# Kernel optimization log

Hardware: AMD Instinct MI355X
Metric: run time of the kernel (lower is better)

Reference implementation:

```python
import jax, jax.numpy as jnp
import numpy as np

B, Q, N, C = 2, 1024, 4096, 768
H, D, REL = 12, 64, 32
SCALE = 1.0 / np.sqrt(D)


def _lin_coords(n_out, n_in):
    # align_corners=True mapping: x_in = x_out * (n_in-1)/(n_out-1)
    pos = jnp.arange(n_out, dtype=jnp.float32) * ((n_in - 1) / (n_out - 1))
    lo = jnp.clip(jnp.floor(pos).astype(jnp.int32), 0, n_in - 1)
    hi = jnp.clip(lo + 1, 0, n_in - 1)
    w = pos - lo.astype(jnp.float32)
    return lo, hi, w


def _interp_bias(bias, q_len, n_len):
    # bias: [H, 32, 32] -> [H, q_len, n_len] bilinear, align_corners=True
    lq, hq, wq = _lin_coords(q_len, REL)
    ln, hn, wn = _lin_coords(n_len, REL)
    b1 = bias[:, lq, :] * (1.0 - wq)[None, :, None] + bias[:, hq, :] * wq[None, :, None]  # [H,q,32]
    b2 = b1[:, :, ln] * (1.0 - wn)[None, None, :] + b1[:, :, hn] * wn[None, None, :]      # [H,q,n]
    return b2


def setup_inputs() -> dict:
    key = jax.random.key(0)
    ks = jax.random.split(key, 11)
    s = 1.0 / np.sqrt(C)
    return {
        "query": jax.random.normal(ks[0], (B, Q, C), jnp.float32),
        "key_value": jax.random.normal(ks[1], (B, N, C), jnp.float32),
        "Wq": jax.random.normal(ks[2], (C, C), jnp.float32) * s,
        "bq": jax.random.normal(ks[3], (C,), jnp.float32) * 0.01,
        "Wk": jax.random.normal(ks[4], (C, C), jnp.float32) * s,
        "bk": jax.random.normal(ks[5], (C,), jnp.float32) * 0.01,
        "Wv": jax.random.normal(ks[6], (C, C), jnp.float32) * s,
        "bv": jax.random.normal(ks[7], (C,), jnp.float32) * 0.01,
        "Wo": jax.random.normal(ks[8], (C, C), jnp.float32) * s,
        "bo": jax.random.normal(ks[9], (C,), jnp.float32) * 0.01,
        "rel_pos_bias": jax.random.normal(ks[10], (H, REL, REL), jnp.float32) * 0.02,
    }


def reference(query, key_value, Wq, bq, Wk, bk, Wv, bv, Wo, bo, rel_pos_bias):
    b, n, c = key_value.shape
    q_len = query.shape[1]
    # projections (dropout in eval mode -> identity)
    q = (query @ Wq + bq).reshape(b, q_len, H, D).transpose(0, 2, 1, 3)      # [B,H,Q,D]
    k = (key_value @ Wk + bk).reshape(b, n, H, D).transpose(0, 2, 1, 3)      # [B,H,N,D]
    v = (key_value @ Wv + bv).reshape(b, n, H, D).transpose(0, 2, 1, 3)      # [B,H,N,D]
    attn = jnp.einsum('bhqd,bhnd->bhqn', q, k) * SCALE
    attn = attn + _interp_bias(rel_pos_bias, q_len, n)[None]                 # [B,H,Q,N]
    p = jax.nn.softmax(attn, axis=-1)
    out = jnp.einsum('bhqn,bhnd->bhqd', p, v)
    out = out.transpose(0, 2, 1, 3).reshape(b, q_len, c)
    return out @ Wo + bo
```

## Files before the change

kernel.cpp:

```cpp
#include <hip/hip_runtime.h>
#include <stdint.h>

typedef unsigned short ushort_t;
typedef __bf16 bf16x8 __attribute__((ext_vector_type(8)));
typedef float f32x4 __attribute__((ext_vector_type(4)));
typedef unsigned short us4 __attribute__((ext_vector_type(4)));

#define LOG2E 1.4426950408889634f
#define NEG8L (-11.541560327111707f)
#define QSCALE 0.18033688011110974f

__device__ __forceinline__ ushort_t f2b(float f) {
    unsigned u = __float_as_uint(f);
    unsigned r = (u + 0x7fffu + ((u >> 16) & 1u)) >> 16;
    return (ushort_t)r;
}
__device__ __forceinline__ void gld16(const void* g, void* l) {
    __builtin_amdgcn_global_load_lds(
        (__attribute__((address_space(1))) void*)g,
        (__attribute__((address_space(3))) void*)l,
        16, 0, 0);
}

__global__ __launch_bounds__(256) void prep(
        const float* __restrict__ query, const float* __restrict__ keyv,
        const float* __restrict__ Wq, const float* __restrict__ Wk,
        const float* __restrict__ Wv, const float* __restrict__ Wo,
        const float* __restrict__ rel,
        ushort_t* __restrict__ qc, ushort_t* __restrict__ kvc,
        ushort_t* __restrict__ wtq, ushort_t* __restrict__ wtk,
        ushort_t* __restrict__ wtv, ushort_t* __restrict__ wto,
        ushort_t* __restrict__ b1b, ushort_t* __restrict__ wtab) {
    __shared__ ushort_t tsh[32][33];
    const int bid = blockIdx.x, tid = threadIdx.x;
    if (bid < 7680) {
        const float* src = (bid < 1536) ? query : keyv;
        ushort_t* dst = (bid < 1536) ? qc : kvc;
        int i = ((bid < 1536) ? bid : bid - 1536) * 256 + tid;
        float4 x = ((const float4*)src)[i];
        us4 v; v.x = f2b(x.x); v.y = f2b(x.y); v.z = f2b(x.z); v.w = f2b(x.w);
        ((us4*)dst)[i] = v;
    } else if (bid < 9984) {
        int t = bid - 7680, w = t / 576, tt = t - w * 576;
        const float* in = (w == 0) ? Wq : (w == 1) ? Wk : (w == 2) ? Wv : Wo;
        ushort_t* out = (w == 0) ? wtq : (w == 1) ? wtk : (w == 2) ? wtv : wto;
        int x = tid & 31, y = tid >> 5;
        int bx = (tt % 24) * 32, by = (tt / 24) * 32;
#pragma unroll
        for (int j = 0; j < 32; j += 8)
            tsh[y + j][x] = f2b(in[(size_t)(by + y + j) * 768 + bx + x]);
        __syncthreads();
#pragma unroll
        for (int j = 0; j < 32; j += 8)
            out[(size_t)(bx + y + j) * 768 + by + x] = tsh[x][y + j];
    } else if (bid < 11520) {
        int idx = (bid - 9984) * 256 + tid;
        int j = idx & 31, q = (idx >> 5) & 1023, h = idx >> 15;
        float pos = q * (31.0f / 1023.0f);
        float fl = floorf(pos);
        int lo = (int)fl; if (lo > 31) lo = 31;
        float w = pos - fl;
        int hi = lo + 1; if (hi > 31) hi = 31;
        float vlo = rel[(h * 32 + lo) * 32 + j];
        float vhi = rel[(h * 32 + hi) * 32 + j];
        b1b[idx] = f2b((vlo + (vhi - vlo) * w) * LOG2E);
    } else {
        int n = (bid - 11520) * 256 + tid;
        float pos = n * (31.0f / 4095.0f);
        float fl = floorf(pos);
        int ln = (int)fl; if (ln > 31) ln = 31;
        float wn = pos - fl;
        int hn = ln + 1; if (hn > 31) hn = 31;
        float vals[32];
#pragma unroll
        for (int j = 0; j < 32; ++j) vals[j] = 0.f;
        vals[ln] += 1.0f - wn;
        vals[hn] += wn;
#pragma unroll
        for (int j = 0; j < 32; ++j) wtab[n * 32 + j] = f2b(vals[j]);
    }
}

template <int MBC>
__device__ __forceinline__ void gemm_body(const ushort_t* __restrict__ A,
                                          const ushort_t* __restrict__ Bt,
                                          const float* __restrict__ bias,
                                          void* __restrict__ out,
                                          int mode, int lsh, float scale,
                                          int m0, int n0,
                                          ushort_t* As, ushort_t* Bs, int tid) {
    const int wave = tid >> 6, lane = tid & 63;
    const int quad = lane >> 4, l15 = lane & 15;
    const f32x4 z4 = {0.f, 0.f, 0.f, 0.f};
    f32x4 acc[MBC][4];
#pragma unroll
    for (int i = 0; i < MBC; ++i)
#pragma unroll
        for (int j = 0; j < 4; ++j) acc[i][j] = z4;

    const int lrow = lane >> 2;
    const int kswz = ((lane & 3) ^ (lrow & 3)) * 8;

    for (int kk = 0; kk < 768; kk += 32) {
        __syncthreads();
#pragma unroll
        for (int i = 0; i < MBC; ++i) {
            int c = wave * MBC + i;
            gld16(A + (size_t)(m0 + c * 16 + lrow) * 768 + kk + kswz, (void*)(As + c * 512));
        }
        gld16(Bt + (size_t)(n0 + wave * 16 + lrow) * 768 + kk + kswz, (void*)(Bs + wave * 512));
        __syncthreads();
        bf16x8 af[MBC], bf[4];
#pragma unroll
        for (int mb = 0; mb < MBC; ++mb) {
            int r = wave * 16 * MBC + mb * 16 + l15;
            af[mb] = *(const bf16x8*)(As + r * 32 + ((quad ^ (r & 3)) * 8));
        }
#pragma unroll
        for (int nb = 0; nb < 4; ++nb) {
            int r = nb * 16 + l15;
            bf[nb] = *(const bf16x8*)(Bs + r * 32 + ((quad ^ (r & 3)) * 8));
        }
#pragma unroll
        for (int mb = 0; mb < MBC; ++mb)
#pragma unroll
            for (int nb = 0; nb < 4; ++nb)
                acc[mb][nb] = __builtin_amdgcn_mfma_f32_16x16x32_bf16(af[mb], bf[nb], acc[mb][nb], 0, 0, 0);
    }

#pragma unroll
    for (int mb = 0; mb < MBC; ++mb) {
        int mbase = m0 + wave * 16 * MBC + mb * 16 + quad * 4;
#pragma unroll
        for (int nb = 0; nb < 4; ++nb) {
            int n = n0 + nb * 16 + l15;
            float bvf = bias[n];
            f32x4 a = acc[mb][nb];
            if (mode == 0) {
#pragma unroll
                for (int r = 0; r < 4; ++r)
                    ((float*)out)[(size_t)(mbase + r) * 768 + n] = (a[r] + bvf) * scale;
            } else if (mode == 1) {
                int h = n >> 6, d = n & 63;
#pragma unroll
                for (int r = 0; r < 4; ++r) {
                    int m = mbase + r;
                    int b = m >> lsh, l = m & ((1 << lsh) - 1);
                    ((ushort_t*)out)[((size_t)(((b * 12 + h) << lsh) + l) << 6) + d] = f2b((a[r] + bvf) * scale);
                }
            } else {
                int h = n >> 6, d = n & 63;
                int b = mbase >> lsh, l = mbase & ((1 << lsh) - 1);
                us4 v;
                v.x = f2b((a[0] + bvf) * scale);
                v.y = f2b((a[1] + bvf) * scale);
                v.z = f2b((a[2] + bvf) * scale);
                v.w = f2b((a[3] + bvf) * scale);
                *(us4*)((ushort_t*)out + ((size_t)((b * 12 + h) * 64 + d) << lsh) + l) = v;
            }
        }
    }
}

__global__ __launch_bounds__(256) void proj3(const ushort_t* __restrict__ qc,
                                             const ushort_t* __restrict__ kvc,
                                             const ushort_t* __restrict__ wtq,
                                             const ushort_t* __restrict__ wtk,
                                             const ushort_t* __restrict__ wtv,
                                             const float* __restrict__ bq,
                                             const float* __restrict__ bk,
                                             const float* __restrict__ bv,
                                             ushort_t* __restrict__ qp,
                                             ushort_t* __restrict__ kp,
                                             ushort_t* __restrict__ vtp) {
    __shared__ __align__(16) ushort_t As[128 * 32];
    __shared__ __align__(16) ushort_t Bs[64 * 32];
    const int bid = blockIdx.x, tid = threadIdx.x;
    if (bid < 384) {
        int mt = bid / 12, nt = bid - mt * 12;
        gemm_body<1>(qc, wtq, bq, qp, 1, 10, QSCALE, mt * 64, nt * 64, As, Bs, tid);
    } else if (bid < 1152) {
        int t = bid - 384, mt = t / 12, nt = t - mt * 12;
        gemm_body<2>(kvc, wtk, bk, kp, 1, 12, 1.0f, mt * 128, nt * 64, As, Bs, tid);
    } else {
        int t = bid - 1152, mt = t / 12, nt = t - mt * 12;
        gemm_body<2>(kvc, wtv, bv, vtp, 2, 12, 1.0f, mt * 128, nt * 64, As, Bs, tid);
    }
}

__global__ __launch_bounds__(256) void gemm_out(const ushort_t* __restrict__ ab,
                                                const ushort_t* __restrict__ wto,
                                                const float* __restrict__ bo,
                                                float* __restrict__ out) {
    __shared__ __align__(16) ushort_t As[64 * 32];
    __shared__ __align__(16) ushort_t Bs[64 * 32];
    const int bid = blockIdx.x, tid = threadIdx.x;
    int mt = bid / 12, nt = bid - mt * 12;
    gemm_body<1>(ab, wto, bo, out, 0, 0, 1.0f, mt * 64, nt * 64, As, Bs, tid);
}

__global__ __launch_bounds__(256) void attn64s(const ushort_t* __restrict__ qp,
                                               const ushort_t* __restrict__ kp,
                                               const ushort_t* __restrict__ vt,
                                               const ushort_t* __restrict__ b1b,
                                               const ushort_t* __restrict__ wtab,
                                               float* __restrict__ po,
                                               float* __restrict__ pl) {
    __shared__ __align__(16) ushort_t k_s[64 * 64];
    __shared__ __align__(16) ushort_t v_s[64 * 64];
    __shared__ __align__(16) float pf[4][576];

    const int tid = threadIdx.x;
    const int wave = tid >> 6, lane = tid & 63;
    const int quad = lane >> 4, l15 = lane & 15;
    const int qt = blockIdx.x, h = blockIdx.y, z = blockIdx.z;
    const int b = z >> 2, sp = z & 3;
    const int q0 = qt * 64;
    const int bh = b * 12 + h;

    const ushort_t* qg = qp + ((size_t)bh * 1024 + q0) * 64;
    const ushort_t* kg = kp + (size_t)bh * 4096 * 64;
    const ushort_t* vg = vt + (size_t)bh * 64 * 4096;

    const int rowq = wave * 16 + l15;
    bf16x8 aq[2];
#pragma unroll
    for (int ks = 0; ks < 2; ++ks)
        aq[ks] = *(const bf16x8*)(qg + (size_t)rowq * 64 + (ks * 4 + quad) * 8);
    bf16x8 ab1 = *(const bf16x8*)(b1b + ((size_t)(h * 1024 + q0 + rowq)) * 32 + quad * 8);

    const f32x4 mC = {NEG8L, NEG8L, NEG8L, NEG8L};
    const f32x4 z4 = {0.f, 0.f, 0.f, 0.f};
    f32x4 o[4];
    float lsum[4];
#pragma unroll
    for (int d = 0; d < 4; ++d) o[d] = z4;
#pragma unroll
    for (int r = 0; r < 4; ++r) lsum[r] = 0.f;

    const int arow = lane >> 3;
    const int ablk = lane & 7;

    for (int nt = 0; nt < 16; ++nt) {
        const int n0 = sp * 1024 + nt * 64;
        __syncthreads();
#pragma unroll
        for (int i = 0; i < 2; ++i) {
            int c = wave * 2 + i;
            int row = c * 8 + arow;
            int k16 = ablk ^ (row & 7);
            gld16(kg + (size_t)(n0 + row) * 64 + k16 * 8, (void*)(k_s + c * 512));
            gld16(vg + (size_t)row * 4096 + n0 + k16 * 8, (void*)(v_s + c * 512));
        }
        __syncthreads();

        bf16x8 wf[4];
#pragma unroll
        for (int nb = 0; nb < 4; ++nb)
            wf[nb] = *(const bf16x8*)(wtab + (size_t)(n0 + nb * 16 + l15) * 32 + quad * 8);

        f32x4 s[4];
#pragma unroll
        for (int nb = 0; nb < 4; ++nb) {
            s[nb] = __builtin_amdgcn_mfma_f32_16x16x32_bf16(ab1, wf[nb], mC, 0, 0, 0);
#pragma unroll
            for (int ks = 0; ks < 2; ++ks) {
                int rn = nb * 16 + l15;
                bf16x8 bk = *(const bf16x8*)(k_s + rn * 64 + (((ks * 4 + quad) ^ (rn & 7)) * 8));
                s[nb] = __builtin_amdgcn_mfma_f32_16x16x32_bf16(aq[ks], bk, s[nb], 0, 0, 0);
            }
        }
#pragma unroll
        for (int nb = 0; nb < 4; ++nb)
#pragma unroll
            for (int r = 0; r < 4; ++r) {
                float p = exp2f(s[nb][r]);
                s[nb][r] = p;
                lsum[r] += p;
            }
#pragma unroll
        for (int p = 0; p < 2; ++p) {
#pragma unroll
            for (int i = 0; i < 2; ++i) {
                int nb = 2 * p + i;
                float* dst = &pf[wave][(i * 16 + l15) * 18 + quad * 4];
                *(float2*)dst = make_float2(s[nb][0], s[nb][1]);
                *(float2*)(dst + 2) = make_float2(s[nb][2], s[nb][3]);
            }
            bf16x8 ap;
#pragma unroll
            for (int j = 0; j < 8; ++j)
                ap[j] = (__bf16)pf[wave][(quad * 8 + j) * 18 + l15];
#pragma unroll
            for (int d = 0; d < 4; ++d) {
                int rd = d * 16 + l15;
                bf16x8 bv = *(const bf16x8*)(v_s + rd * 64 + (((p * 4 + quad) ^ (rd & 7)) * 8));
                o[d] = __builtin_amdgcn_mfma_f32_16x16x32_bf16(ap, bv, o[d], 0, 0, 0);
            }
        }
    }

#pragma unroll
    for (int r = 0; r < 4; ++r)
#pragma unroll
        for (int off = 1; off < 16; off <<= 1)
            lsum[r] += __shfl_xor(lsum[r], off, 64);

    const size_t pbase = ((size_t)(sp * 24 + bh)) * 1024;
#pragma unroll
    for (int r = 0; r < 4; ++r) {
        int qrow = q0 + wave * 16 + quad * 4 + r;
        if (l15 == 0) pl[pbase + qrow] = lsum[r];
#pragma unroll
        for (int d = 0; d < 4; ++d)
            po[(pbase + qrow) * 64 + d * 16 + l15] = o[d][r];
    }
}

__global__ __launch_bounds__(256) void combine(const float* __restrict__ po,
                                               const float* __restrict__ pl,
                                               ushort_t* __restrict__ ab) {
    int idx = blockIdx.x * 256 + threadIdx.x;
    int e = idx * 4;
    int b = e / 786432;
    int rem = e - b * 786432;
    int q = rem / 768;
    int col = rem - q * 768;
    int h = col >> 6, d = col & 63;
    int bh = b * 12 + h;
    float4 acc = {0.f, 0.f, 0.f, 0.f};
    float l = 0.f;
#pragma unroll
    for (int s = 0; s < 4; ++s) {
        size_t base = ((size_t)(s * 24 + bh)) * 1024 + q;
        float4 v = *(const float4*)(po + base * 64 + d);
        acc.x += v.x; acc.y += v.y; acc.z += v.z; acc.w += v.w;
        l += pl[base];
    }
    float inv = 1.0f / l;
    us4 v;
    v.x = f2b(acc.x * inv); v.y = f2b(acc.y * inv);
    v.z = f2b(acc.z * inv); v.w = f2b(acc.w * inv);
    *(us4*)(ab + (size_t)(b * 1024 + q) * 768 + col) = v;
}

extern "C" void kernel_launch(void* const* d_in, const int* in_sizes, int n_in,
                              void* d_out, int out_size, void* d_ws, size_t ws_size,
                              hipStream_t stream) {
    const float* query = (const float*)d_in[0];
    const float* keyv  = (const float*)d_in[1];
    const float* Wq = (const float*)d_in[2];
    const float* bq = (const float*)d_in[3];
    const float* Wk = (const float*)d_in[4];
    const float* bk = (const float*)d_in[5];
    const float* Wv = (const float*)d_in[6];
    const float* bv = (const float*)d_in[7];
    const float* Wo = (const float*)d_in[8];
    const float* bo = (const float*)d_in[9];
    const float* rel = (const float*)d_in[10];

    char* ws = (char*)d_ws;
    ushort_t* qc   = (ushort_t*)(ws + 0);
    ushort_t* kvc  = (ushort_t*)(ws + 3145728);
    ushort_t* wtq  = (ushort_t*)(ws + 15728640);
    ushort_t* wtk  = (ushort_t*)(ws + 16908288);
    ushort_t* wtv  = (ushort_t*)(ws + 18087936);
    ushort_t* wto  = (ushort_t*)(ws + 19267584);
    ushort_t* qp   = (ushort_t*)(ws + 20447232);
    ushort_t* kp   = (ushort_t*)(ws + 23592960);
    ushort_t* vtp  = (ushort_t*)(ws + 36175872);
    ushort_t* b1b  = (ushort_t*)(ws + 48758784);
    ushort_t* wtab = (ushort_t*)(ws + 49545216);
    ushort_t* ab   = (ushort_t*)(ws + 49807360);
    float*    po   = (float*)(ws + 52953088);
    float*    pl   = (float*)(ws + 78118912);

    prep<<<11536, 256, 0, stream>>>(query, keyv, Wq, Wk, Wv, Wo, rel,
                                    qc, kvc, wtq, wtk, wtv, wto, b1b, wtab);
    proj3<<<1920, 256, 0, stream>>>(qc, kvc, wtq, wtk, wtv, bq, bk, bv, qp, kp, vtp);
    attn64s<<<dim3(16, 12, 8), 256, 0, stream>>>(qp, kp, vtp, b1b, wtab, po, pl);
    combine<<<1536, 256, 0, stream>>>(po, pl, ab);
    gemm_out<<<384, 256, 0, stream>>>(ab, wto, bo, (float*)d_out);
}
```

Measured before the change: 232.9 us.

## Enlarge projection and attention tiles to 128 and store P as bf16

```diff
diff --git a/kernel.cpp b/kernel.cpp
--- a/kernel.cpp
+++ b/kernel.cpp
@@ -81,40 +81,117 @@
     }
 }
 
-template <int MBC>
-__device__ __forceinline__ void gemm_body(const ushort_t* __restrict__ A,
-                                          const ushort_t* __restrict__ Bt,
-                                          const float* __restrict__ bias,
-                                          void* __restrict__ out,
-                                          int mode, int lsh, float scale,
-                                          int m0, int n0,
-                                          ushort_t* As, ushort_t* Bs, int tid) {
+__device__ __forceinline__ void gemm_store(float bvf, f32x4 a, void* out,
+                                           int mode, int lsh, float scale,
+                                           int mbase, int n) {
+    if (mode == 0) {
+#pragma unroll
+        for (int r = 0; r < 4; ++r)
+            ((float*)out)[(size_t)(mbase + r) * 768 + n] = (a[r] + bvf) * scale;
+    } else if (mode == 1) {
+        int h = n >> 6, d = n & 63;
+#pragma unroll
+        for (int r = 0; r < 4; ++r) {
+            int m = mbase + r;
+            int b = m >> lsh, l = m & ((1 << lsh) - 1);
+            ((ushort_t*)out)[((size_t)(((b * 12 + h) << lsh) + l) << 6) + d] = f2b((a[r] + bvf) * scale);
+        }
+    } else {
+        int h = n >> 6, d = n & 63;
+        int b = mbase >> lsh, l = mbase & ((1 << lsh) - 1);
+        us4 v;
+        v.x = f2b((a[0] + bvf) * scale);
+        v.y = f2b((a[1] + bvf) * scale);
+        v.z = f2b((a[2] + bvf) * scale);
+        v.w = f2b((a[3] + bvf) * scale);
+        *(us4*)((ushort_t*)out + ((size_t)((b * 12 + h) * 64 + d) << lsh) + l) = v;
+    }
+}
+
+__device__ __forceinline__ void gemm_body128(const ushort_t* __restrict__ A,
+                                             const ushort_t* __restrict__ Bt,
+                                             const float* __restrict__ bias,
+                                             void* __restrict__ out,
+                                             int mode, int lsh, float scale,
+                                             int m0, int n0,
+                                             ushort_t* As, ushort_t* Bs, int tid) {
+    const int wave = tid >> 6, lane = tid & 63;
+    const int quad = lane >> 4, l15 = lane & 15;
+    const int wm = wave >> 1, wn = wave & 1;
+    const f32x4 z4 = {0.f, 0.f, 0.f, 0.f};
+    f32x4 acc[4][4];
+#pragma unroll
+    for (int i = 0; i < 4; ++i)
+#pragma unroll
+        for (int j = 0; j < 4; ++j) acc[i][j] = z4;
+
+    const int lrow = lane >> 2;
+    const int kswz = ((lane & 3) ^ (lrow & 3)) * 8;
+
+    for (int kk = 0; kk < 768; kk += 32) {
+        __syncthreads();
+#pragma unroll
+        for (int i = 0; i < 2; ++i) {
+            int c = wave * 2 + i;
+            gld16(A + (size_t)(m0 + c * 16 + lrow) * 768 + kk + kswz, (void*)(As + c * 512));
+            gld16(Bt + (size_t)(n0 + c * 16 + lrow) * 768 + kk + kswz, (void*)(Bs + c * 512));
+        }
+        __syncthreads();
+        bf16x8 af[4], bf[4];
+#pragma unroll
+        for (int mb = 0; mb < 4; ++mb) {
+            int r = wm * 64 + mb * 16 + l15;
+            af[mb] = *(const bf16x8*)(As + r * 32 + ((quad ^ (r & 3)) * 8));
+        }
+#pragma unroll
+        for (int nb = 0; nb < 4; ++nb) {
+            int r = wn * 64 + nb * 16 + l15;
+            bf[nb] = *(const bf16x8*)(Bs + r * 32 + ((quad ^ (r & 3)) * 8));
+        }
+#pragma unroll
+        for (int mb = 0; mb < 4; ++mb)
+#pragma unroll
+            for (int nb = 0; nb < 4; ++nb)
+                acc[mb][nb] = __builtin_amdgcn_mfma_f32_16x16x32_bf16(af[mb], bf[nb], acc[mb][nb], 0, 0, 0);
+    }
+
+#pragma unroll
+    for (int mb = 0; mb < 4; ++mb) {
+        int mbase = m0 + wm * 64 + mb * 16 + quad * 4;
+#pragma unroll
+        for (int nb = 0; nb < 4; ++nb) {
+            int n = n0 + wn * 64 + nb * 16 + l15;
+            gemm_store(bias[n], acc[mb][nb], out, mode, lsh, scale, mbase, n);
+        }
+    }
+}
+
+__device__ __forceinline__ void gemm_body64(const ushort_t* __restrict__ A,
+                                            const ushort_t* __restrict__ Bt,
+                                            const float* __restrict__ bias,
+                                            void* __restrict__ out,
+                                            int mode, int lsh, float scale,
+                                            int m0, int n0,
+                                            ushort_t* As, ushort_t* Bs, int tid) {
     const int wave = tid >> 6, lane = tid & 63;
     const int quad = lane >> 4, l15 = lane & 15;
     const f32x4 z4 = {0.f, 0.f, 0.f, 0.f};
-    f32x4 acc[MBC][4];
-#pragma unroll
-    for (int i = 0; i < MBC; ++i)
-#pragma unroll
-        for (int j = 0; j < 4; ++j) acc[i][j] = z4;
+    f32x4 acc[4];
+#pragma unroll
+    for (int j = 0; j < 4; ++j) acc[j] = z4;
 
     const int lrow = lane >> 2;
     const int kswz = ((lane & 3) ^ (lrow & 3)) * 8;
 
     for (int kk = 0; kk < 768; kk += 32) {
         __syncthreads();
-#pragma unroll
-        for (int i = 0; i < MBC; ++i) {
-            int c = wave * MBC + i;
-            gld16(A + (size_t)(m0 + c * 16 + lrow) * 768 + kk + kswz, (void*)(As + c * 512));
-        }
+        gld16(A + (size_t)(m0 + wave * 16 + lrow) * 768 + kk + kswz, (void*)(As + wave * 512));
         gld16(Bt + (size_t)(n0 + wave * 16 + lrow) * 768 + kk + kswz, (void*)(Bs + wave * 512));
         __syncthreads();
-        bf16x8 af[MBC], bf[4];
-#pragma unroll
-        for (int mb = 0; mb < MBC; ++mb) {
-            int r = wave * 16 * MBC + mb * 16 + l15;
-            af[mb] = *(const bf16x8*)(As + r * 32 + ((quad ^ (r & 3)) * 8));
+        bf16x8 af, bf[4];
+        {
+            int r = wave * 16 + l15;
+            af = *(const bf16x8*)(As + r * 32 + ((quad ^ (r & 3)) * 8));
         }
 #pragma unroll
         for (int nb = 0; nb < 4; ++nb) {
@@ -122,43 +199,15 @@
             bf[nb] = *(const bf16x8*)(Bs + r * 32 + ((quad ^ (r & 3)) * 8));
         }
 #pragma unroll
-        for (int mb = 0; mb < MBC; ++mb)
-#pragma unroll
-            for (int nb = 0; nb < 4; ++nb)
-                acc[mb][nb] = __builtin_amdgcn_mfma_f32_16x16x32_bf16(af[mb], bf[nb], acc[mb][nb], 0, 0, 0);
-    }
-
-#pragma unroll
-    for (int mb = 0; mb < MBC; ++mb) {
-        int mbase = m0 + wave * 16 * MBC + mb * 16 + quad * 4;
-#pragma unroll
-        for (int nb = 0; nb < 4; ++nb) {
-            int n = n0 + nb * 16 + l15;
-            float bvf = bias[n];
-            f32x4 a = acc[mb][nb];
-            if (mode == 0) {
-#pragma unroll
-                for (int r = 0; r < 4; ++r)
-                    ((float*)out)[(size_t)(mbase + r) * 768 + n] = (a[r] + bvf) * scale;
-            } else if (mode == 1) {
-                int h = n >> 6, d = n & 63;
-#pragma unroll
-                for (int r = 0; r < 4; ++r) {
-                    int m = mbase + r;
-                    int b = m >> lsh, l = m & ((1 << lsh) - 1);
-                    ((ushort_t*)out)[((size_t)(((b * 12 + h) << lsh) + l) << 6) + d] = f2b((a[r] + bvf) * scale);
-                }
-            } else {
-                int h = n >> 6, d = n & 63;
-                int b = mbase >> lsh, l = mbase & ((1 << lsh) - 1);
-                us4 v;
-                v.x = f2b((a[0] + bvf) * scale);
-                v.y = f2b((a[1] + bvf) * scale);
-                v.z = f2b((a[2] + bvf) * scale);
-                v.w = f2b((a[3] + bvf) * scale);
-                *(us4*)((ushort_t*)out + ((size_t)((b * 12 + h) * 64 + d) << lsh) + l) = v;
-            }
-        }
+        for (int nb = 0; nb < 4; ++nb)
+            acc[nb] = __builtin_amdgcn_mfma_f32_16x16x32_bf16(af, bf[nb], acc[nb], 0, 0, 0);
+    }
+
+    int mbase = m0 + wave * 16 + quad * 4;
+#pragma unroll
+    for (int nb = 0; nb < 4; ++nb) {
+        int n = n0 + nb * 16 + l15;
+        gemm_store(bias[n], acc[nb], out, mode, lsh, scale, mbase, n);
     }
 }
 
@@ -174,17 +223,17 @@
                                              ushort_t* __restrict__ kp,
                                              ushort_t* __restrict__ vtp) {
     __shared__ __align__(16) ushort_t As[128 * 32];
-    __shared__ __align__(16) ushort_t Bs[64 * 32];
+    __shared__ __align__(16) ushort_t Bs[128 * 32];
     const int bid = blockIdx.x, tid = threadIdx.x;
-    if (bid < 384) {
-        int mt = bid / 12, nt = bid - mt * 12;
-        gemm_body<1>(qc, wtq, bq, qp, 1, 10, QSCALE, mt * 64, nt * 64, As, Bs, tid);
-    } else if (bid < 1152) {
-        int t = bid - 384, mt = t / 12, nt = t - mt * 12;
-        gemm_body<2>(kvc, wtk, bk, kp, 1, 12, 1.0f, mt * 128, nt * 64, As, Bs, tid);
+    if (bid < 96) {
+        int mt = bid / 6, nt = bid - mt * 6;
+        gemm_body128(qc, wtq, bq, qp, 1, 10, QSCALE, mt * 128, nt * 128, As, Bs, tid);
+    } else if (bid < 480) {
+        int t = bid - 96, mt = t / 6, nt = t - mt * 6;
+        gemm_body128(kvc, wtk, bk, kp, 1, 12, 1.0f, mt * 128, nt * 128, As, Bs, tid);
     } else {
-        int t = bid - 1152, mt = t / 12, nt = t - mt * 12;
-        gemm_body<2>(kvc, wtv, bv, vtp, 2, 12, 1.0f, mt * 128, nt * 64, As, Bs, tid);
+        int t = bid - 480, mt = t / 6, nt = t - mt * 6;
+        gemm_body128(kvc, wtv, bv, vtp, 2, 12, 1.0f, mt * 128, nt * 128, As, Bs, tid);
     }
 }
 
@@ -196,10 +245,10 @@
     __shared__ __align__(16) ushort_t Bs[64 * 32];
     const int bid = blockIdx.x, tid = threadIdx.x;
     int mt = bid / 12, nt = bid - mt * 12;
-    gemm_body<1>(ab, wto, bo, out, 0, 0, 1.0f, mt * 64, nt * 64, As, Bs, tid);
-}
-
-__global__ __launch_bounds__(256) void attn64s(const ushort_t* __restrict__ qp,
+    gemm_body64(ab, wto, bo, out, 0, 0, 1.0f, mt * 64, nt * 64, As, Bs, tid);
+}
+
+__global__ __launch_bounds__(256) void attn128(const ushort_t* __restrict__ qp,
                                                const ushort_t* __restrict__ kp,
                                                const ushort_t* __restrict__ vt,
                                                const ushort_t* __restrict__ b1b,
@@ -208,113 +257,124 @@
                                                float* __restrict__ pl) {
     __shared__ __align__(16) ushort_t k_s[64 * 64];
     __shared__ __align__(16) ushort_t v_s[64 * 64];
-    __shared__ __align__(16) float pf[4][576];
+    __shared__ __align__(16) __bf16 pb[4][2][16 * 72];
 
     const int tid = threadIdx.x;
     const int wave = tid >> 6, lane = tid & 63;
     const int quad = lane >> 4, l15 = lane & 15;
     const int qt = blockIdx.x, h = blockIdx.y, z = blockIdx.z;
     const int b = z >> 2, sp = z & 3;
-    const int q0 = qt * 64;
+    const int q0 = qt * 128;
     const int bh = b * 12 + h;
 
     const ushort_t* qg = qp + ((size_t)bh * 1024 + q0) * 64;
     const ushort_t* kg = kp + (size_t)bh * 4096 * 64;
     const ushort_t* vg = vt + (size_t)bh * 64 * 4096;
 
-    const int rowq = wave * 16 + l15;
-    bf16x8 aq[2];
-#pragma unroll
-    for (int ks = 0; ks < 2; ++ks)
-        aq[ks] = *(const bf16x8*)(qg + (size_t)rowq * 64 + (ks * 4 + quad) * 8);
-    bf16x8 ab1 = *(const bf16x8*)(b1b + ((size_t)(h * 1024 + q0 + rowq)) * 32 + quad * 8);
+    bf16x8 aq[2][2], ab1[2];
+#pragma unroll
+    for (int rb = 0; rb < 2; ++rb) {
+        int rowq = rb * 64 + wave * 16 + l15;
+#pragma unroll
+        for (int ks = 0; ks < 2; ++ks)
+            aq[rb][ks] = *(const bf16x8*)(qg + (size_t)rowq * 64 + (ks * 4 + quad) * 8);
+        ab1[rb] = *(const bf16x8*)(b1b + ((size_t)(h * 1024 + q0 + rowq)) * 32 + quad * 8);
+    }
 
     const f32x4 mC = {NEG8L, NEG8L, NEG8L, NEG8L};
     const f32x4 z4 = {0.f, 0.f, 0.f, 0.f};
-    f32x4 o[4];
-    float lsum[4];
-#pragma unroll
-    for (int d = 0; d < 4; ++d) o[d] = z4;
-#pragma unroll
-    for (int r = 0; r < 4; ++r) lsum[r] = 0.f;
+    f32x4 o[2][4];
+    float lsum[2][4];
+#pragma unroll
+    for (int rb = 0; rb < 2; ++rb) {
+#pragma unroll
+        for (int d = 0; d < 4; ++d) o[rb][d] = z4;
+#pragma unroll
+        for (int r = 0; r < 4; ++r) lsum[rb][r] = 0.f;
+    }
 
     const int arow = lane >> 3;
     const int ablk = lane & 7;
+    const int c0 = wave * 2, c1 = wave * 2 + 1;
+    const ushort_t* kptr0 = kg + (size_t)(sp * 1024 + c0 * 8 + arow) * 64 + (ablk ^ ((c0 * 8 + arow) & 7)) * 8;
+    const ushort_t* kptr1 = kg + (size_t)(sp * 1024 + c1 * 8 + arow) * 64 + (ablk ^ ((c1 * 8 + arow) & 7)) * 8;
+    const ushort_t* vptr0 = vg + (size_t)(c0 * 8 + arow) * 4096 + sp * 1024 + (ablk ^ ((c0 * 8 + arow) & 7)) * 8;
+    const ushort_t* vptr1 = vg + (size_t)(c1 * 8 + arow) * 4096 + sp * 1024 + (ablk ^ ((c1 * 8 + arow) & 7)) * 8;
+    const ushort_t* wptr = wtab + (size_t)(sp * 1024) * 32 + l15 * 32 + quad * 8;
 
     for (int nt = 0; nt < 16; ++nt) {
-        const int n0 = sp * 1024 + nt * 64;
-        __syncthreads();
-#pragma unroll
-        for (int i = 0; i < 2; ++i) {
-            int c = wave * 2 + i;
-            int row = c * 8 + arow;
-            int k16 = ablk ^ (row & 7);
-            gld16(kg + (size_t)(n0 + row) * 64 + k16 * 8, (void*)(k_s + c * 512));
-            gld16(vg + (size_t)row * 4096 + n0 + k16 * 8, (void*)(v_s + c * 512));
-        }
+        __syncthreads();
+        gld16(kptr0, (void*)(k_s + c0 * 512));
+        gld16(kptr1, (void*)(k_s + c1 * 512));
+        gld16(vptr0, (void*)(v_s + c0 * 512));
+        gld16(vptr1, (void*)(v_s + c1 * 512));
+        kptr0 += 4096; kptr1 += 4096; vptr0 += 64; vptr1 += 64;
         __syncthreads();
 
         bf16x8 wf[4];
 #pragma unroll
         for (int nb = 0; nb < 4; ++nb)
-            wf[nb] = *(const bf16x8*)(wtab + (size_t)(n0 + nb * 16 + l15) * 32 + quad * 8);
-
-        f32x4 s[4];
+            wf[nb] = *(const bf16x8*)(wptr + nb * 512);
+        wptr += 2048;
+
+        f32x4 s0[4], s1[4];
 #pragma unroll
         for (int nb = 0; nb < 4; ++nb) {
-            s[nb] = __builtin_amdgcn_mfma_f32_16x16x32_bf16(ab1, wf[nb], mC, 0, 0, 0);
+            s0[nb] = __builtin_amdgcn_mfma_f32_16x16x32_bf16(ab1[0], wf[nb], mC, 0, 0, 0);
+            s1[nb] = __builtin_amdgcn_mfma_f32_16x16x32_bf16(ab1[1], wf[nb], mC, 0, 0, 0);
+            int rn = nb * 16 + l15;
 #pragma unroll
             for (int ks = 0; ks < 2; ++ks) {
-                int rn = nb * 16 + l15;
                 bf16x8 bk = *(const bf16x8*)(k_s + rn * 64 + (((ks * 4 + quad) ^ (rn & 7)) * 8));
-                s[nb] = __builtin_amdgcn_mfma_f32_16x16x32_bf16(aq[ks], bk, s[nb], 0, 0, 0);
+                s0[nb] = __builtin_amdgcn_mfma_f32_16x16x32_bf16(aq[0][ks], bk, s0[nb], 0, 0, 0);
+                s1[nb] = __builtin_amdgcn_mfma_f32_16x16x32_bf16(aq[1][ks], bk, s1[nb], 0, 0, 0);
             }
         }
 #pragma unroll
-        for (int nb = 0; nb < 4; ++nb)
+        for (int nb = 0; nb < 4; ++nb) {
 #pragma unroll
             for (int r = 0; r < 4; ++r) {
-                float p = exp2f(s[nb][r]);
-                s[nb][r] = p;
-                lsum[r] += p;
+                float p0 = exp2f(s0[nb][r]);
+                float p1 = exp2f(s1[nb][r]);
+                lsum[0][r] += p0;
+                lsum[1][r] += p1;
+                pb[wave][0][(quad * 4 + r) * 72 + nb * 16 + l15] = (__bf16)p0;
+                pb[wave][1][(quad * 4 + r) * 72 + nb * 16 + l15] = (__bf16)p1;
             }
+        }
 #pragma unroll
         for (int p = 0; p < 2; ++p) {
-#pragma unroll
-            for (int i = 0; i < 2; ++i) {
-                int nb = 2 * p + i;
-                float* dst = &pf[wave][(i * 16 + l15) * 18 + quad * 4];
-                *(float2*)dst = make_float2(s[nb][0], s[nb][1]);
-                *(float2*)(dst + 2) = make_float2(s[nb][2], s[nb][3]);
-            }
-            bf16x8 ap;
-#pragma unroll
-            for (int j = 0; j < 8; ++j)
-                ap[j] = (__bf16)pf[wave][(quad * 8 + j) * 18 + l15];
+            bf16x8 ap0 = *(const bf16x8*)&pb[wave][0][l15 * 72 + p * 32 + quad * 8];
+            bf16x8 ap1 = *(const bf16x8*)&pb[wave][1][l15 * 72 + p * 32 + quad * 8];
 #pragma unroll
             for (int d = 0; d < 4; ++d) {
                 int rd = d * 16 + l15;
                 bf16x8 bv = *(const bf16x8*)(v_s + rd * 64 + (((p * 4 + quad) ^ (rd & 7)) * 8));
-                o[d] = __builtin_amdgcn_mfma_f32_16x16x32_bf16(ap, bv, o[d], 0, 0, 0);
+                o[0][d] = __builtin_amdgcn_mfma_f32_16x16x32_bf16(ap0, bv, o[0][d], 0, 0, 0);
+                o[1][d] = __builtin_amdgcn_mfma_f32_16x16x32_bf16(ap1, bv, o[1][d], 0, 0, 0);
             }
         }
     }
 
 #pragma unroll
-    for (int r = 0; r < 4; ++r)
-#pragma unroll
-        for (int off = 1; off < 16; off <<= 1)
-            lsum[r] += __shfl_xor(lsum[r], off, 64);
+    for (int rb = 0; rb < 2; ++rb)
+#pragma unroll
+        for (int r = 0; r < 4; ++r)
+#pragma unroll
+            for (int off = 1; off < 16; off <<= 1)
+                lsum[rb][r] += __shfl_xor(lsum[rb][r], off, 64);
 
     const size_t pbase = ((size_t)(sp * 24 + bh)) * 1024;
 #pragma unroll
-    for (int r = 0; r < 4; ++r) {
-        int qrow = q0 + wave * 16 + quad * 4 + r;
-        if (l15 == 0) pl[pbase + qrow] = lsum[r];
-#pragma unroll
-        for (int d = 0; d < 4; ++d)
-            po[(pbase + qrow) * 64 + d * 16 + l15] = o[d][r];
-    }
+    for (int rb = 0; rb < 2; ++rb)
+#pragma unroll
+        for (int r = 0; r < 4; ++r) {
+            int qrow = q0 + rb * 64 + wave * 16 + quad * 4 + r;
+            if (l15 == 0) pl[pbase + qrow] = lsum[rb][r];
+#pragma unroll
+            for (int d = 0; d < 4; ++d)
+                po[(pbase + qrow) * 64 + d * 16 + l15] = o[rb][d][r];
+        }
 }
 
 __global__ __launch_bounds__(256) void combine(const float* __restrict__ po,
@@ -377,8 +437,8 @@
 
     prep<<<11536, 256, 0, stream>>>(query, keyv, Wq, Wk, Wv, Wo, rel,
                                     qc, kvc, wtq, wtk, wtv, wto, b1b, wtab);
-    proj3<<<1920, 256, 0, stream>>>(qc, kvc, wtq, wtk, wtv, bq, bk, bv, qp, kp, vtp);
-    attn64s<<<dim3(16, 12, 8), 256, 0, stream>>>(qp, kp, vtp, b1b, wtab, po, pl);
+    proj3<<<864, 256, 0, stream>>>(qc, kvc, wtq, wtk, wtv, bq, bk, bv, qp, kp, vtp);
+    attn128<<<dim3(8, 12, 8), 256, 0, stream>>>(qp, kp, vtp, b1b, wtab, po, pl);
     combine<<<1536, 256, 0, stream>>>(po, pl, ab);
     gemm_out<<<384, 256, 0, stream>>>(ab, wto, bo, (float*)d_out);
 }
```

Result: slower. 243.7 us (+4.6%).

## Enlarge projection GEMM tiles to 128x128 and deepen K step to 64

Applied to the files above, without the earlier changes.

```diff
diff --git a/kernel.cpp b/kernel.cpp
--- a/kernel.cpp
+++ b/kernel.cpp
@@ -81,84 +81,145 @@
     }
 }
 
-template <int MBC>
-__device__ __forceinline__ void gemm_body(const ushort_t* __restrict__ A,
-                                          const ushort_t* __restrict__ Bt,
-                                          const float* __restrict__ bias,
-                                          void* __restrict__ out,
-                                          int mode, int lsh, float scale,
-                                          int m0, int n0,
-                                          ushort_t* As, ushort_t* Bs, int tid) {
+__device__ __forceinline__ void gemm_store(float bvf, f32x4 a, void* out,
+                                           int mode, int lsh, float scale,
+                                           int mbase, int n) {
+    if (mode == 0) {
+#pragma unroll
+        for (int r = 0; r < 4; ++r)
+            ((float*)out)[(size_t)(mbase + r) * 768 + n] = (a[r] + bvf) * scale;
+    } else if (mode == 1) {
+        int h = n >> 6, d = n & 63;
+#pragma unroll
+        for (int r = 0; r < 4; ++r) {
+            int m = mbase + r;
+            int b = m >> lsh, l = m & ((1 << lsh) - 1);
+            ((ushort_t*)out)[((size_t)(((b * 12 + h) << lsh) + l) << 6) + d] = f2b((a[r] + bvf) * scale);
+        }
+    } else {
+        int h = n >> 6, d = n & 63;
+        int b = mbase >> lsh, l = mbase & ((1 << lsh) - 1);
+        us4 v;
+        v.x = f2b((a[0] + bvf) * scale);
+        v.y = f2b((a[1] + bvf) * scale);
+        v.z = f2b((a[2] + bvf) * scale);
+        v.w = f2b((a[3] + bvf) * scale);
+        *(us4*)((ushort_t*)out + ((size_t)((b * 12 + h) * 64 + d) << lsh) + l) = v;
+    }
+}
+
+__device__ __forceinline__ void gemm_body128(const ushort_t* __restrict__ A,
+                                             const ushort_t* __restrict__ Bt,
+                                             const float* __restrict__ bias,
+                                             void* __restrict__ out,
+                                             int mode, int lsh, float scale,
+                                             int m0, int n0,
+                                             ushort_t* As, ushort_t* Bs, int tid) {
+    const int wave = tid >> 6, lane = tid & 63;
+    const int quad = lane >> 4, l15 = lane & 15;
+    const int wm = wave >> 1, wn = wave & 1;
+    const f32x4 z4 = {0.f, 0.f, 0.f, 0.f};
+    f32x4 acc[4][4];
+#pragma unroll
+    for (int i = 0; i < 4; ++i)
+#pragma unroll
+        for (int j = 0; j < 4; ++j) acc[i][j] = z4;
+
+    const int arow = lane >> 3;
+    const int ablk = lane & 7;
+    const int kswz = (ablk ^ arow) * 8;
+
+    for (int kk = 0; kk < 768; kk += 64) {
+        __syncthreads();
+#pragma unroll
+        for (int i = 0; i < 4; ++i) {
+            int c = wave * 4 + i;
+            gld16(A + (size_t)(m0 + c * 8 + arow) * 768 + kk + kswz, (void*)(As + c * 512));
+            gld16(Bt + (size_t)(n0 + c * 8 + arow) * 768 + kk + kswz, (void*)(Bs + c * 512));
+        }
+        __syncthreads();
+#pragma unroll
+        for (int ks = 0; ks < 2; ++ks) {
+            bf16x8 af[4], bf[4];
+#pragma unroll
+            for (int mb = 0; mb < 4; ++mb) {
+                int r = wm * 64 + mb * 16 + l15;
+                af[mb] = *(const bf16x8*)(As + r * 64 + (((ks * 4 + quad) ^ (r & 7)) * 8));
+            }
+#pragma unroll
+            for (int nb = 0; nb < 4; ++nb) {
+                int r = wn * 64 + nb * 16 + l15;
+                bf[nb] = *(const bf16x8*)(Bs + r * 64 + (((ks * 4 + quad) ^ (r & 7)) * 8));
+            }
+#pragma unroll
+            for (int mb = 0; mb < 4; ++mb)
+#pragma unroll
+                for (int nb = 0; nb < 4; ++nb)
+                    acc[mb][nb] = __builtin_amdgcn_mfma_f32_16x16x32_bf16(af[mb], bf[nb], acc[mb][nb], 0, 0, 0);
+        }
+    }
+
+#pragma unroll
+    for (int mb = 0; mb < 4; ++mb) {
+        int mbase = m0 + wm * 64 + mb * 16 + quad * 4;
+#pragma unroll
+        for (int nb = 0; nb < 4; ++nb) {
+            int n = n0 + wn * 64 + nb * 16 + l15;
+            gemm_store(bias[n], acc[mb][nb], out, mode, lsh, scale, mbase, n);
+        }
+    }
+}
+
+__device__ __forceinline__ void gemm_body64(const ushort_t* __restrict__ A,
+                                            const ushort_t* __restrict__ Bt,
+                                            const float* __restrict__ bias,
+                                            void* __restrict__ out,
+                                            int mode, int lsh, float scale,
+                                            int m0, int n0,
+                                            ushort_t* As, ushort_t* Bs, int tid) {
     const int wave = tid >> 6, lane = tid & 63;
     const int quad = lane >> 4, l15 = lane & 15;
     const f32x4 z4 = {0.f, 0.f, 0.f, 0.f};
-    f32x4 acc[MBC][4];
-#pragma unroll
-    for (int i = 0; i < MBC; ++i)
-#pragma unroll
-        for (int j = 0; j < 4; ++j) acc[i][j] = z4;
-
-    const int lrow = lane >> 2;
-    const int kswz = ((lane & 3) ^ (lrow & 3)) * 8;
-
-    for (int kk = 0; kk < 768; kk += 32) {
-        __syncthreads();
-#pragma unroll
-        for (int i = 0; i < MBC; ++i) {
-            int c = wave * MBC + i;
-            gld16(A + (size_t)(m0 + c * 16 + lrow) * 768 + kk + kswz, (void*)(As + c * 512));
-        }
-        gld16(Bt + (size_t)(n0 + wave * 16 + lrow) * 768 + kk + kswz, (void*)(Bs + wave * 512));
-        __syncthreads();
-        bf16x8 af[MBC], bf[4];
-#pragma unroll
-        for (int mb = 0; mb < MBC; ++mb) {
-            int r = wave * 16 * MBC + mb * 16 + l15;
-            af[mb] = *(const bf16x8*)(As + r * 32 + ((quad ^ (r & 3)) * 8));
-        }
-#pragma unroll
-        for (int nb = 0; nb < 4; ++nb) {
-            int r = nb * 16 + l15;
-            bf[nb] = *(const bf16x8*)(Bs + r * 32 + ((quad ^ (r & 3)) * 8));
-        }
-#pragma unroll
-        for (int mb = 0; mb < MBC; ++mb)
+    f32x4 acc[4];
+#pragma unroll
+    for (int j = 0; j < 4; ++j) acc[j] = z4;
+
+    const int arow = lane >> 3;
+    const int ablk = lane & 7;
+    const int kswz = (ablk ^ arow) * 8;
+
+    for (int kk = 0; kk < 768; kk += 64) {
+        __syncthreads();
+#pragma unroll
+        for (int i = 0; i < 2; ++i) {
+            int c = wave * 2 + i;
+            gld16(A + (size_t)(m0 + c * 8 + arow) * 768 + kk + kswz, (void*)(As + c * 512));
+            gld16(Bt + (size_t)(n0 + c * 8 + arow) * 768 + kk + kswz, (void*)(Bs + c * 512));
+        }
+        __syncthreads();
+#pragma unroll
+        for (int ks = 0; ks < 2; ++ks) {
+            bf16x8 af, bf[4];
+            {
+                int r = wave * 16 + l15;
+                af = *(const bf16x8*)(As + r * 64 + (((ks * 4 + quad) ^ (r & 7)) * 8));
+            }
+#pragma unroll
+            for (int nb = 0; nb < 4; ++nb) {
+                int r = nb * 16 + l15;
+                bf[nb] = *(const bf16x8*)(Bs + r * 64 + (((ks * 4 + quad) ^ (r & 7)) * 8));
+            }
 #pragma unroll
             for (int nb = 0; nb < 4; ++nb)
-                acc[mb][nb] = __builtin_amdgcn_mfma_f32_16x16x32_bf16(af[mb], bf[nb], acc[mb][nb], 0, 0, 0);
-    }
-
-#pragma unroll
-    for (int mb = 0; mb < MBC; ++mb) {
-        int mbase = m0 + wave * 16 * MBC + mb * 16 + quad * 4;
-#pragma unroll
-        for (int nb = 0; nb < 4; ++nb) {
-            int n = n0 + nb * 16 + l15;
-            float bvf = bias[n];
-            f32x4 a = acc[mb][nb];
-            if (mode == 0) {
-#pragma unroll
-                for (int r = 0; r < 4; ++r)
-                    ((float*)out)[(size_t)(mbase + r) * 768 + n] = (a[r] + bvf) * scale;
-            } else if (mode == 1) {
-                int h = n >> 6, d = n & 63;
-#pragma unroll
-                for (int r = 0; r < 4; ++r) {
-                    int m = mbase + r;
-                    int b = m >> lsh, l = m & ((1 << lsh) - 1);
-                    ((ushort_t*)out)[((size_t)(((b * 12 + h) << lsh) + l) << 6) + d] = f2b((a[r] + bvf) * scale);
-                }
-            } else {
-                int h = n >> 6, d = n & 63;
-                int b = mbase >> lsh, l = mbase & ((1 << lsh) - 1);
-                us4 v;
-                v.x = f2b((a[0] + bvf) * scale);
-                v.y = f2b((a[1] + bvf) * scale);
-                v.z = f2b((a[2] + bvf) * scale);
-                v.w = f2b((a[3] + bvf) * scale);
-                *(us4*)((ushort_t*)out + ((size_t)((b * 12 + h) * 64 + d) << lsh) + l) = v;
-            }
-        }
+                acc[nb] = __builtin_amdgcn_mfma_f32_16x16x32_bf16(af, bf[nb], acc[nb], 0, 0, 0);
+        }
+    }
+
+    int mbase = m0 + wave * 16 + quad * 4;
+#pragma unroll
+    for (int nb = 0; nb < 4; ++nb) {
+        int n = n0 + nb * 16 + l15;
+        gemm_store(bias[n], acc[nb], out, mode, lsh, scale, mbase, n);
     }
 }
 
@@ -173,18 +234,18 @@
                                              ushort_t* __restrict__ qp,
                                              ushort_t* __restrict__ kp,
                                              ushort_t* __restrict__ vtp) {
-    __shared__ __align__(16) ushort_t As[128 * 32];
-    __shared__ __align__(16) ushort_t Bs[64 * 32];
+    __shared__ __align__(16) ushort_t As[128 * 64];
+    __shared__ __align__(16) ushort_t Bs[128 * 64];
     const int bid = blockIdx.x, tid = threadIdx.x;
-    if (bid < 384) {
-        int mt = bid / 12, nt = bid - mt * 12;
-        gemm_body<1>(qc, wtq, bq, qp, 1, 10, QSCALE, mt * 64, nt * 64, As, Bs, tid);
-    } else if (bid < 1152) {
-        int t = bid - 384, mt = t / 12, nt = t - mt * 12;
-        gemm_body<2>(kvc, wtk, bk, kp, 1, 12, 1.0f, mt * 128, nt * 64, As, Bs, tid);
+    if (bid < 96) {
+        int mt = bid / 6, nt = bid - mt * 6;
+        gemm_body128(qc, wtq, bq, qp, 1, 10, QSCALE, mt * 128, nt * 128, As, Bs, tid);
+    } else if (bid < 480) {
+        int t = bid - 96, mt = t / 6, nt = t - mt * 6;
+        gemm_body128(kvc, wtk, bk, kp, 1, 12, 1.0f, mt * 128, nt * 128, As, Bs, tid);
     } else {
-        int t = bid - 1152, mt = t / 12, nt = t - mt * 12;
-        gemm_body<2>(kvc, wtv, bv, vtp, 2, 12, 1.0f, mt * 128, nt * 64, As, Bs, tid);
+        int t = bid - 480, mt = t / 6, nt = t - mt * 6;
+        gemm_body128(kvc, wtv, bv, vtp, 2, 12, 1.0f, mt * 128, nt * 128, As, Bs, tid);
     }
 }
 
@@ -192,11 +253,11 @@
                                                 const ushort_t* __restrict__ wto,
                                                 const float* __restrict__ bo,
                                                 float* __restrict__ out) {
-    __shared__ __align__(16) ushort_t As[64 * 32];
-    __shared__ __align__(16) ushort_t Bs[64 * 32];
+    __shared__ __align__(16) ushort_t As[64 * 64];
+    __shared__ __align__(16) ushort_t Bs[64 * 64];
     const int bid = blockIdx.x, tid = threadIdx.x;
     int mt = bid / 12, nt = bid - mt * 12;
-    gemm_body<1>(ab, wto, bo, out, 0, 0, 1.0f, mt * 64, nt * 64, As, Bs, tid);
+    gemm_body64(ab, wto, bo, out, 0, 0, 1.0f, mt * 64, nt * 64, As, Bs, tid);
 }
 
 __global__ __launch_bounds__(256) void attn64s(const ushort_t* __restrict__ qp,
@@ -377,7 +438,7 @@
 
     prep<<<11536, 256, 0, stream>>>(query, keyv, Wq, Wk, Wv, Wo, rel,
                                     qc, kvc, wtq, wtk, wtv, wto, b1b, wtab);
-    proj3<<<1920, 256, 0, stream>>>(qc, kvc, wtq, wtk, wtv, bq, bk, bv, qp, kp, vtp);
+    proj3<<<864, 256, 0, stream>>>(qc, kvc, wtq, wtk, wtv, bq, bk, bv, qp, kp, vtp);
     attn64s<<<dim3(16, 12, 8), 256, 0, stream>>>(qp, kp, vtp, b1b, wtab, po, pl);
     combine<<<1536, 256, 0, stream>>>(po, pl, ab);
     gemm_out<<<384, 256, 0, stream>>>(ab, wto, bo, (float*)d_out);
```

Measured after the change: 222.2 us. 4.6% less time.
